# Kernel optimization log

Measured on AMD Instinct MI355X. Metric: run time of the kernel, lower is better.

## Reference

```python
import jax, jax.numpy as jnp
import numpy as np
from itertools import product

L0 = (41, 1600, 1408)  # sparse_shape (z,y,x) from pc_range / voxel_size + [1,0,0]
B = 4
N_PER = 25000
PNAMES = ['w_in','s_in','b_in','w1','s1','b1','w2a','s2a','b2a','w2b','s2b','b2b','w2c','s2c','b2c','w3a','s3a','b3a','w3b','s3b','b3b','w3c','s3c','b3c','w4a','s4a','b4a','w4b','s4b','b4b','w4c','s4c','b4c','w_out','s_out','b_out']


def _enc(c, shape):
    D, H, W = shape
    return ((c[:, 0].astype(np.int64) * D + c[:, 1]) * H + c[:, 2]) * W + c[:, 3]


def _subm_rb(coords, shape):
    # submanifold conv rulebook: out site i gathers input j with coord_j = coord_i + offset
    N = coords.shape[0]
    keys = _enc(coords, shape)
    order = np.argsort(keys); sk = keys[order]
    ins, outs = [], []
    for dz, dy, dx in product((-1, 0, 1), repeat=3):
        nb = coords.astype(np.int64).copy()
        nb[:, 1] += dz; nb[:, 2] += dy; nb[:, 3] += dx
        ok = ((nb[:, 1] >= 0) & (nb[:, 1] < shape[0]) & (nb[:, 2] >= 0) & (nb[:, 2] < shape[1]) & (nb[:, 3] >= 0) & (nb[:, 3] < shape[2]))
        qi = np.nonzero(ok)[0]
        qk = _enc(nb[qi], shape)
        pos = np.clip(np.searchsorted(sk, qk), 0, N - 1)
        f = sk[pos] == qk
        ins.append(order[pos[f]].astype(np.int32))
        outs.append(qi[f].astype(np.int32))
    R = max(len(a) for a in ins)
    rin = np.zeros((27, R), np.int32); rout = np.full((27, R), N, np.int32)  # pad -> dummy out row
    for k in range(27):
        rin[k, :len(ins[k])] = ins[k]; rout[k, :len(outs[k])] = outs[k]
    return jnp.asarray(rin), jnp.asarray(rout)


def _spconv_rb(coords, shape, ks, st, pd):
    # strided sparse conv: out = (in + pad - k) / stride where divisible and in-bounds
    osh = tuple((shape[i] + 2 * pd[i] - ks[i]) // st[i] + 1 for i in range(3))
    per = []; allk = []
    for off in product(*[range(k) for k in ks]):
        oc = np.empty((coords.shape[0], 4), np.int64)
        oc[:, 0] = coords[:, 0]
        ok = np.ones(coords.shape[0], bool)
        for d in range(3):
            v = coords[:, d + 1].astype(np.int64) + pd[d] - off[d]
            ok &= (v % st[d] == 0)
            v = v // st[d]
            ok &= (v >= 0) & (v < osh[d])
            oc[:, d + 1] = v
        qi = np.nonzero(ok)[0]
        qk = _enc(oc[qi], osh)
        per.append((qi.astype(np.int32), qk)); allk.append(qk)
    uk = np.unique(np.concatenate(allk))
    Nout = len(uk); K = len(per)
    R = max(len(qi) for qi, _ in per)
    rin = np.zeros((K, R), np.int32); rout = np.full((K, R), Nout, np.int32)
    for k, (qi, qk) in enumerate(per):
        rin[k, :len(qi)] = qi
        rout[k, :len(qi)] = np.searchsorted(uk, qk).astype(np.int32)
    t = uk.copy()
    x = t % osh[2]; t //= osh[2]; y = t % osh[1]; t //= osh[1]; z = t % osh[0]; b = t // osh[0]
    ocoords = np.stack([b, z, y, x], 1).astype(np.int32)
    return jnp.asarray(rin), jnp.asarray(rout), ocoords, osh


def _gen_coords(rng):
    # clustered LiDAR-like voxel occupancy: gaussian clusters so 3x3x3 neighborhoods are populated
    out = []
    for b in range(B):
        nc = 250
        ctr = np.stack([rng.integers(6, 34, nc), rng.integers(60, 1540, nc), rng.integers(60, 1348, nc)], 1)
        pts = ctr[np.repeat(np.arange(nc), 400)] + rng.normal(0.0, 2.0, (nc * 400, 3))
        pts = np.rint(pts).astype(np.int64)
        for d in range(3):
            pts[:, d] = np.clip(pts[:, d], 0, L0[d] - 1)
        keys = (pts[:, 0] * L0[1] + pts[:, 1]) * L0[2] + pts[:, 2]
        _, ui = np.unique(keys, return_index=True)
        assert len(ui) >= N_PER
        c = pts[np.sort(ui[:N_PER])]
        out.append(np.concatenate([np.full((N_PER, 1), b, np.int64), c], 1))
    return np.concatenate(out, 0).astype(np.int32)


def _conv(feat, W, rin, rout, nout):
    # gather -> per-offset GEMM -> scatter-add (spconv rulebook algorithm)
    out = jnp.zeros((nout + 1, W.shape[2]), feat.dtype)  # +1 dummy row for padding
    for k in range(W.shape[0]):
        out = out.at[rout[k]].add(feat[rin[k]] @ W[k])
    return out[:nout]


def _bnrelu(x, s, b):
    # eval-mode BatchNorm1d folded to affine, then ReLU
    return jax.nn.relu(x * s + b)


def _net(voxels, normalizer, rb1_in, rb1_out, rb2s_in, rb2s_out, batch2, rb2_in, rb2_out, rb3s_in, rb3s_out, batch3, rb3_in, rb3_out, rb4s_in, rb4s_out, batch4, rb4_in, rb4_out, rbo_in, rbo_out, batch_out, P):
    n0 = voxels.shape[0]; n2 = batch2.shape[0]; n3 = batch3.shape[0]; n4 = batch4.shape[0]; no = batch_out.shape[0]
    f = voxels.sum(1) / normalizer  # mean VFE: (N0, 4)
    x = _bnrelu(_conv(f, P['w_in'], rb1_in, rb1_out, n0), P['s_in'], P['b_in'])
    x = _bnrelu(_conv(x, P['w1'], rb1_in, rb1_out, n0), P['s1'], P['b1'])
    x = _bnrelu(_conv(x, P['w2a'], rb2s_in, rb2s_out, n2), P['s2a'], P['b2a'])
    x = _bnrelu(_conv(x, P['w2b'], rb2_in, rb2_out, n2), P['s2b'], P['b2b'])
    x = _bnrelu(_conv(x, P['w2c'], rb2_in, rb2_out, n2), P['s2c'], P['b2c'])
    x = _bnrelu(_conv(x, P['w3a'], rb3s_in, rb3s_out, n3), P['s3a'], P['b3a'])
    x = _bnrelu(_conv(x, P['w3b'], rb3_in, rb3_out, n3), P['s3b'], P['b3b'])
    x = _bnrelu(_conv(x, P['w3c'], rb3_in, rb3_out, n3), P['s3c'], P['b3c'])
    x = _bnrelu(_conv(x, P['w4a'], rb4s_in, rb4s_out, n4), P['s4a'], P['b4a'])
    x = _bnrelu(_conv(x, P['w4b'], rb4_in, rb4_out, n4), P['s4b'], P['b4b'])
    x = _bnrelu(_conv(x, P['w4c'], rb4_in, rb4_out, n4), P['s4c'], P['b4c'])
    x = _bnrelu(_conv(x, P['w_out'], rbo_in, rbo_out, no), P['s_out'], P['b_out'])
    # per-batch global max pool over active voxels (== F.max_pool1d over voxel dim)
    return jax.ops.segment_max(x, batch_out.astype(jnp.int32), num_segments=B)


def setup_inputs():
    rng = np.random.default_rng(0)
    coords0 = _gen_coords(rng)
    rb1_in, rb1_out = _subm_rb(coords0, L0)
    rb2s_in, rb2s_out, c2, sh2 = _spconv_rb(coords0, L0, (3, 3, 3), (2, 2, 2), (1, 1, 1))
    rb2_in, rb2_out = _subm_rb(c2, sh2)
    rb3s_in, rb3s_out, c3, sh3 = _spconv_rb(c2, sh2, (3, 3, 3), (2, 2, 2), (1, 1, 1))
    rb3_in, rb3_out = _subm_rb(c3, sh3)
    rb4s_in, rb4s_out, c4, sh4 = _spconv_rb(c3, sh3, (3, 3, 3), (2, 2, 2), (0, 1, 1))
    rb4_in, rb4_out = _subm_rb(c4, sh4)
    rbo_in, rbo_out, co, _ = _spconv_rb(c4, sh4, (3, 1, 1), (2, 1, 1), (0, 0, 0))
    N0 = coords0.shape[0]
    d = dict(
        voxels=jnp.asarray(rng.normal(0, 1, (N0, 5, 4)).astype(np.float32)),
        voxel_num_points=jnp.asarray(rng.integers(1, 6, N0).astype(np.int32)),
        voxel_coords=jnp.asarray(coords0),
        rb1_in=rb1_in, rb1_out=rb1_out,
        rb2s_in=rb2s_in, rb2s_out=rb2s_out, batch2=jnp.asarray(c2[:, 0]),
        rb2_in=rb2_in, rb2_out=rb2_out,
        rb3s_in=rb3s_in, rb3s_out=rb3s_out, batch3=jnp.asarray(c3[:, 0]),
        rb3_in=rb3_in, rb3_out=rb3_out,
        rb4s_in=rb4s_in, rb4s_out=rb4s_out, batch4=jnp.asarray(c4[:, 0]),
        rb4_in=rb4_in, rb4_out=rb4_out,
        rbo_in=rbo_in, rbo_out=rbo_out, batch_out=jnp.asarray(co[:, 0]),
    )
    def _w(k, ci, co_):
        return jnp.asarray((rng.normal(0, 1, (k, ci, co_)) / np.sqrt(k * ci)).astype(np.float32))
    def _bn(c):
        return (jnp.asarray(rng.uniform(0.5, 1.5, c).astype(np.float32)), jnp.asarray(rng.normal(0, 0.1, c).astype(np.float32)))
    d['w_in'] = _w(27, 4, 16); d['s_in'], d['b_in'] = _bn(16)
    d['w1'] = _w(27, 16, 16); d['s1'], d['b1'] = _bn(16)
    d['w2a'] = _w(27, 16, 32); d['s2a'], d['b2a'] = _bn(32)
    d['w2b'] = _w(27, 32, 32); d['s2b'], d['b2b'] = _bn(32)
    d['w2c'] = _w(27, 32, 32); d['s2c'], d['b2c'] = _bn(32)
    d['w3a'] = _w(27, 32, 64); d['s3a'], d['b3a'] = _bn(64)
    d['w3b'] = _w(27, 64, 64); d['s3b'], d['b3b'] = _bn(64)
    d['w3c'] = _w(27, 64, 64); d['s3c'], d['b3c'] = _bn(64)
    d['w4a'] = _w(27, 64, 64); d['s4a'], d['b4a'] = _bn(64)
    d['w4b'] = _w(27, 64, 64); d['s4b'], d['b4b'] = _bn(64)
    d['w4c'] = _w(27, 64, 64); d['s4c'], d['b4c'] = _bn(64)
    d['w_out'] = _w(3, 64, 128); d['s_out'], d['b_out'] = _bn(128)
    return d


def reference(voxels, voxel_num_points, voxel_coords, rb1_in, rb1_out, rb2s_in, rb2s_out, batch2, rb2_in, rb2_out, rb3s_in, rb3s_out, batch3, rb3_in, rb3_out, rb4s_in, rb4s_out, batch4, rb4_in, rb4_out, rbo_in, rbo_out, batch_out, w_in, s_in, b_in, w1, s1, b1, w2a, s2a, b2a, w2b, s2b, b2b, w2c, s2c, b2c, w3a, s3a, b3a, w3b, s3b, b3b, w3c, s3c, b3c, w4a, s4a, b4a, w4b, s4b, b4b, w4c, s4c, b4c, w_out, s_out, b_out):
    normalizer = jnp.maximum(voxel_num_points.astype(voxels.dtype), 1.0)[:, None]
    P = dict(zip(PNAMES, (w_in, s_in, b_in, w1, s1, b1, w2a, s2a, b2a, w2b, s2b, b2b, w2c, s2c, b2c, w3a, s3a, b3a, w3b, s3b, b3b, w3c, s3c, b3c, w4a, s4a, b4a, w4b, s4b, b4b, w4c, s4c, b4c, w_out, s_out, b_out)))
    return _net(voxels, normalizer, rb1_in, rb1_out, rb2s_in, rb2s_out, batch2, rb2_in, rb2_out, rb3s_in, rb3s_out, batch3, rb3_in, rb3_out, rb4s_in, rb4s_out, batch4, rb4_in, rb4_out, rbo_in, rbo_out, batch_out, P)
```

## Files before the change

kernel.cpp:

```cpp
#include <hip/hip_runtime.h>
#include <cstddef>
#include <cstdint>

typedef _Float16 half8 __attribute__((ext_vector_type(8)));
typedef float floatx4 __attribute__((ext_vector_type(4)));

static inline int cdiv_i(int a, int b) { return (a + b - 1) / b; }

__global__ void feat_kernel(const float* __restrict__ vox,
                            const int* __restrict__ vnp,
                            _Float16* __restrict__ f, int N0) {
  int t = blockIdx.x * blockDim.x + threadIdx.x;
  if (t >= (N0 + 1) * 8) return;
  int i = t >> 3, c = t & 7;
  float v = 0.f;
  if (i < N0 && c < 4) {
    const float* p = vox + (size_t)i * 20 + c;
    v = (p[0] + p[4] + p[8] + p[12] + p[16]) / fmaxf((float)vnp[i], 1.f);
  }
  f[t] = (_Float16)v;
}

struct RB { const int* rin; const int* rout; int K, R, nout, start, end, off; };
struct RBs { RB d[8]; };
__global__ void rb_fill_all(RBs P, int* __restrict__ tbl, int total) {
  int idx = blockIdx.x * blockDim.x + threadIdx.x;
  if (idx >= total) return;
#pragma unroll
  for (int l = 0; l < 8; ++l) {
    if (idx >= P.d[l].start && idx < P.d[l].end) {
      const RB rb = P.d[l];
      int e = idx - rb.start;
      int o = rb.rout[e];
      if ((unsigned)o < (unsigned)rb.nout) {
        int k = e / rb.R;
        tbl[rb.off + (size_t)k * rb.nout + o] = rb.rin[e];
      }
    }
  }
}

__global__ void tbl_fill_kernel(const int* __restrict__ rin,
                                const int* __restrict__ rout,
                                int* __restrict__ tbl, int K, int R, int nout) {
  int e = blockIdx.x * blockDim.x + threadIdx.x;
  if (e >= K * R) return;
  int o = rout[e];
  if ((unsigned)o >= (unsigned)nout) return;
  int k = e / R;
  tbl[(size_t)k * nout + o] = rin[e];
}

struct WP { const float* W; int K, Ci, CiPad, Co, start, end, off; };
struct WPs { WP d[12]; };
__global__ void wpack_all(WPs P, _Float16* __restrict__ Bp, int total) {
  int idx = blockIdx.x * blockDim.x + threadIdx.x;
  if (idx >= total) return;
#pragma unroll
  for (int l = 0; l < 12; ++l) {
    if (idx >= P.d[l].start && idx < P.d[l].end) {
      const WP w = P.d[l];
      int e = idx - w.start;
      int j = e & 7;
      int lane = (e >> 3) & 63;
      int rest = e >> 9;
      int NT = w.Co >> 4;
      int t = rest % NT, ch = rest / NT;
      int kk = ch * 32 + ((lane >> 4) << 3) + j;
      int k = kk / w.CiPad, ci = kk % w.CiPad;
      int n = t * 16 + (lane & 15);
      float v = (k < w.K && ci < w.Ci)
                    ? w.W[((size_t)k * w.Ci + ci) * w.Co + n]
                    : 0.f;
      Bp[w.off + e] = (_Float16)v;
    }
  }
}

template <int K, int CiPad, int Co, int KS, int CG, int CBLK>
__global__ __launch_bounds__(256) void conv_mfma(
    const _Float16* __restrict__ feat, const _Float16* __restrict__ Bp,
    const int* __restrict__ tbl, const float* __restrict__ sc,
    const float* __restrict__ bi, _Float16* __restrict__ out,
    int nout, int nin) {
  constexpr int NT = Co / 16;
  constexpr int NTE = NT / CBLK;
  constexpr int NTW = NTE / CG;
  constexpr int RG = 4 / (KS * CG);
  static_assert(KS * CG * RG == 4 && RG >= 1 && NT % CBLK == 0 && NTE % CG == 0);
  constexpr int DIV = (CiPad >= 32) ? (CiPad / 32) : 1;
  constexpr int NCH = (K * CiPad + 31) / 32;
  constexpr int L2C = (CiPad == 8) ? 3 : 4;
  constexpr int CoP = NTE * 16 + 4;

  __shared__ float red[(KS > 1) ? (KS - 1) * RG * 16 * CoP : 1];

  if (blockIdx.x == 0 && threadIdx.x < Co)
    out[(size_t)nout * Co + threadIdx.x] = (_Float16)0.f;

  int id = blockIdx.x;
  {
    int nb = gridDim.x, nb8 = (nb >> 3) << 3;
    if (id < nb8) {
      int per = nb >> 3;
      id = (id & 7) * per + (id >> 3);
    }
  }
  const int rt = id / CBLK, cb = id % CBLK;

  const int wave = threadIdx.x >> 6, lane = threadIdx.x & 63;
  const int ks = wave % KS;
  const int cg = (wave / KS) % CG;
  const int rowg = wave / (KS * CG);
  const int m = lane & 15, lb = (lane >> 4) * 8;
  const int i0 = (rt * RG + rowg) * 16;
  if constexpr (KS == 1) {
    if (i0 >= nout) return;
  }
  const int row = i0 + m;
  const bool rOK = row < nout;
  const int ct0 = cb * NTE + cg * NTW;

  floatx4 acc[NTW];
#pragma unroll
  for (int n = 0; n < NTW; ++n) {
    floatx4 z = {0.f, 0.f, 0.f, 0.f};
    acc[n] = z;
  }

  if constexpr (CiPad >= 32) {
    constexpr int NKW = (K + KS - 1) / KS;
    constexpr int NC = NKW * DIV;
    constexpr int DA = NC < 8 ? NC : 8;
    constexpr int DB = NC < 2 ? NC : 2;
    int idx[NKW];
#pragma unroll
    for (int q = 0; q < NKW; ++q) {
      int k = ks + q * KS;
      int jj = (rOK && k < K) ? tbl[(size_t)k * nout + row] : -1;
      idx[q] = (jj < 0) ? nin : jj;
    }
    half8 ap[DA];
    half8 bq[DB][NTW];
#pragma unroll
    for (int d = 0; d < DA; ++d)
      ap[d] = *(const half8*)(feat + (size_t)idx[d / DIV] * CiPad +
                              (d % DIV) * 32 + lb);
#pragma unroll
    for (int d = 0; d < DB; ++d) {
      int k = ks + (d / DIV) * KS;
      int ch = ((k < K) ? k : (K - 1)) * DIV + (d % DIV);
#pragma unroll
      for (int n = 0; n < NTW; ++n)
        bq[d][n] = *(const half8*)(Bp + ((size_t)ch * NT * 64 + lane) * 8 +
                                   (size_t)(ct0 + n) * 512);
    }
#pragma unroll
    for (int ii = 0; ii < NC; ++ii) {
      half8 a = ap[ii % DA];
      half8 bt[NTW];
#pragma unroll
      for (int n = 0; n < NTW; ++n) bt[n] = bq[ii % DB][n];
      if (ii + DA < NC) {
        int nx = ii + DA;
        ap[ii % DA] = *(const half8*)(feat + (size_t)idx[nx / DIV] * CiPad +
                                      (nx % DIV) * 32 + lb);
      }
      if (ii + DB < NC) {
        int nx = ii + DB;
        int k = ks + (nx / DIV) * KS;
        int ch = ((k < K) ? k : (K - 1)) * DIV + (nx % DIV);
#pragma unroll
        for (int n = 0; n < NTW; ++n)
          bq[ii % DB][n] = *(const half8*)(Bp + ((size_t)ch * NT * 64 + lane) * 8 +
                                           (size_t)(ct0 + n) * 512);
      }
#pragma unroll
      for (int n = 0; n < NTW; ++n)
        acc[n] = __builtin_amdgcn_mfma_f32_16x16x32_f16(a, bt[n], acc[n], 0, 0, 0);
    }
  } else {
    constexpr int NCW = (NCH + KS - 1) / KS;
    constexpr int DA = NCW < 8 ? NCW : 8;
    constexpr int DB = NCW < 2 ? NCW : 2;
    int idx[NCW];
#pragma unroll
    for (int q = 0; q < NCW; ++q) {
      int ch = ks + q * KS;
      int ko = (ch * 32 + lb) >> L2C;
      int jj = (rOK && ko < K && ch < NCH) ? tbl[(size_t)ko * nout + row] : -1;
      idx[q] = (jj < 0) ? nin : jj;
    }
    half8 ap[DA];
    half8 bq[DB][NTW];
#pragma unroll
    for (int d = 0; d < DA; ++d) {
      int ch = ks + d * KS;
      ap[d] = *(const half8*)(feat + (size_t)idx[d] * CiPad +
                              ((ch * 32 + lb) & (CiPad - 1)));
    }
#pragma unroll
    for (int d = 0; d < DB; ++d) {
      int ch = ks + d * KS;
      if (ch >= NCH) ch = NCH - 1;
#pragma unroll
      for (int n = 0; n < NTW; ++n)
        bq[d][n] = *(const half8*)(Bp + ((size_t)ch * NT * 64 + lane) * 8 +
                                   (size_t)(ct0 + n) * 512);
    }
#pragma unroll
    for (int ii = 0; ii < NCW; ++ii) {
      half8 a = ap[ii % DA];
      half8 bt[NTW];
#pragma unroll
      for (int n = 0; n < NTW; ++n) bt[n] = bq[ii % DB][n];
      if (ii + DA < NCW) {
        int nx = ii + DA;
        int ch = ks + nx * KS;
        ap[ii % DA] = *(const half8*)(feat + (size_t)idx[nx] * CiPad +
                                      ((ch * 32 + lb) & (CiPad - 1)));
      }
      if (ii + DB < NCW) {
        int nx = ii + DB;
        int ch = ks + nx * KS;
        if (ch >= NCH) ch = NCH - 1;
#pragma unroll
        for (int n = 0; n < NTW; ++n)
          bq[ii % DB][n] = *(const half8*)(Bp + ((size_t)ch * NT * 64 + lane) * 8 +
                                           (size_t)(ct0 + n) * 512);
      }
#pragma unroll
      for (int n = 0; n < NTW; ++n)
        acc[n] = __builtin_amdgcn_mfma_f32_16x16x32_f16(a, bt[n], acc[n], 0, 0, 0);
    }
  }

  const int rl = (lane >> 4) * 4;
  if constexpr (KS > 1) {
    if (ks > 0) {
#pragma unroll
      for (int n = 0; n < NTW; ++n) {
        int lcol = (cg * NTW + n) * 16 + m;
#pragma unroll
        for (int r = 0; r < 4; ++r)
          red[((ks - 1) * RG + rowg) * 16 * CoP + (rl + r) * CoP + lcol] = acc[n][r];
      }
    }
    __syncthreads();
    if (ks > 0) return;
#pragma unroll
    for (int s = 1; s < KS; ++s)
#pragma unroll
      for (int n = 0; n < NTW; ++n) {
        int lcol = (cg * NTW + n) * 16 + m;
#pragma unroll
        for (int r = 0; r < 4; ++r)
          acc[n][r] += red[((s - 1) * RG + rowg) * 16 * CoP + (rl + r) * CoP + lcol];
      }
  }

#pragma unroll
  for (int n = 0; n < NTW; ++n) {
    int col = (ct0 + n) * 16 + m;
    float s_ = sc[col], b_ = bi[col];
#pragma unroll
    for (int r = 0; r < 4; ++r) {
      int orow = i0 + rl + r;
      if (orow < nout)
        out[(size_t)orow * Co + col] = (_Float16)fmaxf(fmaf(acc[n][r], s_, b_), 0.f);
    }
  }
}

__global__ __launch_bounds__(256) void segmax2(const _Float16* __restrict__ x,
                                               const int* __restrict__ batch,
                                               int n, float* __restrict__ out) {
  const int RPB = 128;
  int c = threadIdx.x & 127, g = threadIdx.x >> 7;
  int r0 = blockIdx.x * RPB + g;
  int rend = min(n, blockIdx.x * RPB + RPB);
  float mx = 0.f;
  int cb = -1;
  for (int r = r0; r < rend; r += 2) {
    int b = batch[r];
    if (b != cb) {
      if (cb >= 0)
        atomicMax((int*)out + ((size_t)cb << 7) + c, __float_as_int(mx));
      cb = b;
      mx = 0.f;
    }
    mx = fmaxf(mx, (float)x[(size_t)r * 128 + c]);
  }
  if (cb >= 0)
    atomicMax((int*)out + ((size_t)cb << 7) + c, __float_as_int(mx));
}

extern "C" void kernel_launch(void* const* d_in, const int* in_sizes, int n_in,
                              void* d_out, int out_size, void* d_ws, size_t ws_size,
                              hipStream_t stream) {
  auto I = [&](int idx) { return (const int*)d_in[idx]; };
  auto F = [&](int idx) { return (const float*)d_in[idx]; };

  const int N0  = in_sizes[1];
  const int R1  = in_sizes[3] / 27;
  const int R2s = in_sizes[5] / 27;
  const int n2  = in_sizes[7];
  const int R2  = in_sizes[8] / 27;
  const int R3s = in_sizes[10] / 27;
  const int n3  = in_sizes[12];
  const int R3  = in_sizes[13] / 27;
  const int R4s = in_sizes[15] / 27;
  const int n4  = in_sizes[17];
  const int R4  = in_sizes[18] / 27;
  const int Ro  = in_sizes[20] / 3;
  const int no  = in_sizes[22];

  const int wIdx[12] = {23, 26, 29, 32, 35, 38, 41, 44, 47, 50, 53, 56};
  const int Ks[12]   = {27, 27, 27, 27, 27, 27, 27, 27, 27, 27, 27, 3};
  const int Cis[12]  = {4, 16, 16, 32, 32, 32, 64, 64, 64, 64, 64, 64};
  const int Cos[12]  = {16, 16, 32, 32, 32, 64, 64, 64, 64, 64, 64, 128};
  WPs P;
  int wtot = 0;
  int bpOff[12];
  for (int l = 0; l < 12; ++l) {
    int cip = Cis[l] < 8 ? 8 : Cis[l];
    int nch = (Ks[l] * cip + 31) / 32;
    int nt = Cos[l] / 16;
    int sz = nch * nt * 512;
    P.d[l].W = F(wIdx[l]);
    P.d[l].K = Ks[l];  P.d[l].Ci = Cis[l];  P.d[l].CiPad = cip;  P.d[l].Co = Cos[l];
    P.d[l].start = wtot;  P.d[l].end = wtot + sz;  P.d[l].off = wtot;
    bpOff[l] = wtot;
    wtot += sz;
  }

  RBs RP;
  const int rbRin[8]  = {3, 5, 8, 10, 13, 15, 18, 20};
  const int rbRs[8]   = {R1, R2s, R2, R3s, R3, R4s, R4, Ro};
  const int rbKs[8]   = {27, 27, 27, 27, 27, 27, 27, 3};
  const int rbNout[8] = {N0, n2, n2, n3, n3, n4, n4, no};
  size_t tblInts[8], tblOff[8];
  size_t totTbl = 0;
  int totFill = 0;
  for (int l = 0; l < 8; ++l) {
    tblInts[l] = (size_t)rbNout[l] * rbKs[l];
    tblOff[l] = totTbl;
    totTbl += tblInts[l];
    RP.d[l].rin = I(rbRin[l]);
    RP.d[l].rout = I(rbRin[l] + 1);
    RP.d[l].K = rbKs[l];  RP.d[l].R = rbRs[l];  RP.d[l].nout = rbNout[l];
    RP.d[l].start = totFill;
    totFill += rbKs[l] * rbRs[l];
    RP.d[l].end = totFill;
    RP.d[l].off = (int)tblOff[l];
  }

  size_t S = (size_t)(N0 + 1) * 16;
  auto smax = [&](size_t v) { if (v > S) S = v; };
  smax((size_t)(n2 + 1) * 32);
  smax((size_t)(n3 + 1) * 64);
  smax((size_t)(n4 + 1) * 64);
  smax((size_t)(no + 1) * 128);
  S = (S + 7) & ~(size_t)7;

  _Float16* h = (_Float16*)d_ws;
  size_t off = 0;
  _Float16* f0 = h + off;   off += (size_t)(N0 + 1) * 8;
  _Float16* bufA = h + off; off += S;
  _Float16* bufB = h + off; off += S;
  _Float16* Bp = h + off;   off += (size_t)((wtot + 7) & ~7);
  int* tblBase = (int*)(h + off);
  size_t usedBytes = off * 2;
  bool prebuilt = (usedBytes + totTbl * 4 <= ws_size);

  feat_kernel<<<cdiv_i((N0 + 1) * 8, 256), 256, 0, stream>>>(F(0), I(1), f0, N0);
  wpack_all<<<cdiv_i(wtot, 256), 256, 0, stream>>>(P, Bp, wtot);
  hipMemsetAsync(d_out, 0, (size_t)out_size * 4, stream);

  const int l2rb[12] = {0, 0, 1, 2, 2, 3, 4, 4, 5, 6, 6, 7};
  const int* tblL[12];
  if (prebuilt) {
    hipMemsetAsync(tblBase, 0xFF, totTbl * 4, stream);
    rb_fill_all<<<cdiv_i(totFill, 256), 256, 0, stream>>>(RP, tblBase, totFill);
    for (int l = 0; l < 12; ++l) tblL[l] = tblBase + tblOff[l2rb[l]];
  } else {
    for (int l = 0; l < 12; ++l) tblL[l] = tblBase;
  }
  auto buildSeq = [&](int rb) {
    if (prebuilt) return;
    hipMemsetAsync(tblBase, 0xFF, tblInts[rb] * 4, stream);
    tbl_fill_kernel<<<cdiv_i(rbKs[rb] * rbRs[rb], 256), 256, 0, stream>>>(
        I(rbRin[rb]), I(rbRin[rb] + 1), tblBase, rbKs[rb], rbRs[rb], rbNout[rb]);
  };

#define CONV(Kk, CIP, CO, KSv, CGv, CBv, IN, LI, OUTB, NOUT, NIN)             \
  do {                                                                        \
    constexpr int rowsPerBlk = (4 / (KSv * CGv)) * 16;                        \
    int nblk = cdiv_i(NOUT, rowsPerBlk) * CBv;                                \
    conv_mfma<Kk, CIP, CO, KSv, CGv, CBv>                                     \
        <<<nblk, 256, 0, stream>>>(                                           \
            IN, Bp + bpOff[LI], tblL[LI], F(wIdx[LI] + 1), F(wIdx[LI] + 2),   \
            OUTB, NOUT, NIN);                                                 \
  } while (0)

  buildSeq(0);
  CONV(27, 8, 16, 1, 1, 1, f0, 0, bufA, N0, N0);
  CONV(27, 16, 16, 2, 1, 1, bufA, 1, bufB, N0, N0);
  buildSeq(1);
  CONV(27, 16, 32, 2, 1, 1, bufB, 2, bufA, n2, N0);
  buildSeq(2);
  CONV(27, 32, 32, 2, 1, 1, bufA, 3, bufB, n2, n2);
  CONV(27, 32, 32, 2, 1, 1, bufB, 4, bufA, n2, n2);
  buildSeq(3);
  CONV(27, 32, 64, 4, 1, 1, bufA, 5, bufB, n3, n2);
  buildSeq(4);
  CONV(27, 64, 64, 4, 1, 1, bufB, 6, bufA, n3, n3);
  CONV(27, 64, 64, 4, 1, 1, bufA, 7, bufB, n3, n3);
  buildSeq(5);
  CONV(27, 64, 64, 4, 1, 2, bufB, 8, bufA, n4, n3);
  buildSeq(6);
  CONV(27, 64, 64, 4, 1, 2, bufA, 9, bufB, n4, n4);
  CONV(27, 64, 64, 4, 1, 2, bufB, 10, bufA, n4, n4);
  buildSeq(7);
  CONV(3, 64, 128, 2, 2, 2, bufA, 11, bufB, no, n4);
  segmax2<<<cdiv_i(no, 128), 256, 0, stream>>>(bufB, I(22), no, (float*)d_out);
#undef CONV
}
```

Measured before the change: 448.2 us.

## Use 32x32x16 MFMA conv kernel with repacked weights for mid layers

Adds a conv_mfma32 kernel that uses 32x32x16 f16 MFMA tiles (32 rows per wave) plus a matching 32-column weight packing, and switches layers 3-10 to it with new K-split/column-group configurations. Larger MFMA tiles raise arithmetic per loaded A/B fragment and cut the number of instructions per output. In exchange they use more accumulator registers and LDS for the K-split reduction, and give coarser row tiles on sparse row counts.

After: 451.2 us. No clear change (+0.7%).

```diff
diff --git a/kernel.cpp b/kernel.cpp
--- a/kernel.cpp
+++ b/kernel.cpp
@@ -4,6 +4,7 @@
 
 typedef _Float16 half8 __attribute__((ext_vector_type(8)));
 typedef float floatx4 __attribute__((ext_vector_type(4)));
+typedef float floatx16 __attribute__((ext_vector_type(16)));
 
 static inline int cdiv_i(int a, int b) { return (a + b - 1) / b; }
 
@@ -51,7 +52,7 @@
   tbl[(size_t)k * nout + o] = rin[e];
 }
 
-struct WP { const float* W; int K, Ci, CiPad, Co, start, end, off; };
+struct WP { const float* W; int K, Ci, CiPad, Co, start, end, off, p32; };
 struct WPs { WP d[12]; };
 __global__ void wpack_all(WPs P, _Float16* __restrict__ Bp, int total) {
   int idx = blockIdx.x * blockDim.x + threadIdx.x;
@@ -64,14 +65,23 @@
       int j = e & 7;
       int lane = (e >> 3) & 63;
       int rest = e >> 9;
-      int NT = w.Co >> 4;
-      int t = rest % NT, ch = rest / NT;
-      int kk = ch * 32 + ((lane >> 4) << 3) + j;
-      int k = kk / w.CiPad, ci = kk % w.CiPad;
-      int n = t * 16 + (lane & 15);
-      float v = (k < w.K && ci < w.Ci)
-                    ? w.W[((size_t)k * w.Ci + ci) * w.Co + n]
-                    : 0.f;
+      float v;
+      if (w.p32) {
+        int NT = w.Co >> 5;
+        int t = rest % NT, ch = rest / NT;
+        int SUB = w.CiPad >> 4;
+        int ko = ch / SUB, s = ch % SUB;
+        int ci = s * 16 + ((lane >> 5) << 3) + j;
+        int col = t * 32 + (lane & 31);
+        v = w.W[((size_t)ko * w.Ci + ci) * w.Co + col];
+      } else {
+        int NT = w.Co >> 4;
+        int t = rest % NT, ch = rest / NT;
+        int kk = ch * 32 + ((lane >> 4) << 3) + j;
+        int k = kk / w.CiPad, ci = kk % w.CiPad;
+        int n = t * 16 + (lane & 15);
+        v = (k < w.K && ci < w.Ci) ? w.W[((size_t)k * w.Ci + ci) * w.Co + n] : 0.f;
+      }
       Bp[w.off + e] = (_Float16)v;
     }
   }
@@ -88,9 +98,9 @@
   constexpr int NTW = NTE / CG;
   constexpr int RG = 4 / (KS * CG);
   static_assert(KS * CG * RG == 4 && RG >= 1 && NT % CBLK == 0 && NTE % CG == 0);
-  constexpr int DIV = (CiPad >= 32) ? (CiPad / 32) : 1;
   constexpr int NCH = (K * CiPad + 31) / 32;
   constexpr int L2C = (CiPad == 8) ? 3 : 4;
+  constexpr int DIV = (CiPad >= 32) ? (CiPad / 32) : 1;
   constexpr int CoP = NTE * 16 + 4;
 
   __shared__ float red[(KS > 1) ? (KS - 1) * RG * 16 * CoP : 1];
@@ -99,34 +109,23 @@
     out[(size_t)nout * Co + threadIdx.x] = (_Float16)0.f;
 
   int id = blockIdx.x;
-  {
-    int nb = gridDim.x, nb8 = (nb >> 3) << 3;
-    if (id < nb8) {
-      int per = nb >> 3;
-      id = (id & 7) * per + (id >> 3);
-    }
-  }
+  { int nb = gridDim.x, nb8 = (nb >> 3) << 3;
+    if (id < nb8) { int per = nb >> 3; id = (id & 7) * per + (id >> 3); } }
   const int rt = id / CBLK, cb = id % CBLK;
-
   const int wave = threadIdx.x >> 6, lane = threadIdx.x & 63;
   const int ks = wave % KS;
   const int cg = (wave / KS) % CG;
   const int rowg = wave / (KS * CG);
   const int m = lane & 15, lb = (lane >> 4) * 8;
   const int i0 = (rt * RG + rowg) * 16;
-  if constexpr (KS == 1) {
-    if (i0 >= nout) return;
-  }
+  if constexpr (KS == 1) { if (i0 >= nout) return; }
   const int row = i0 + m;
   const bool rOK = row < nout;
   const int ct0 = cb * NTE + cg * NTW;
 
   floatx4 acc[NTW];
 #pragma unroll
-  for (int n = 0; n < NTW; ++n) {
-    floatx4 z = {0.f, 0.f, 0.f, 0.f};
-    acc[n] = z;
-  }
+  for (int n = 0; n < NTW; ++n) { floatx4 z = {0,0,0,0}; acc[n] = z; }
 
   if constexpr (CiPad >= 32) {
     constexpr int NKW = (K + KS - 1) / KS;
@@ -140,12 +139,10 @@
       int jj = (rOK && k < K) ? tbl[(size_t)k * nout + row] : -1;
       idx[q] = (jj < 0) ? nin : jj;
     }
-    half8 ap[DA];
-    half8 bq[DB][NTW];
+    half8 ap[DA]; half8 bq[DB][NTW];
 #pragma unroll
     for (int d = 0; d < DA; ++d)
-      ap[d] = *(const half8*)(feat + (size_t)idx[d / DIV] * CiPad +
-                              (d % DIV) * 32 + lb);
+      ap[d] = *(const half8*)(feat + (size_t)idx[d / DIV] * CiPad + (d % DIV) * 32 + lb);
 #pragma unroll
     for (int d = 0; d < DB; ++d) {
       int k = ks + (d / DIV) * KS;
@@ -191,13 +188,11 @@
       int jj = (rOK && ko < K && ch < NCH) ? tbl[(size_t)ko * nout + row] : -1;
       idx[q] = (jj < 0) ? nin : jj;
     }
-    half8 ap[DA];
-    half8 bq[DB][NTW];
+    half8 ap[DA]; half8 bq[DB][NTW];
 #pragma unroll
     for (int d = 0; d < DA; ++d) {
       int ch = ks + d * KS;
-      ap[d] = *(const half8*)(feat + (size_t)idx[d] * CiPad +
-                              ((ch * 32 + lb) & (CiPad - 1)));
+      ap[d] = *(const half8*)(feat + (size_t)idx[d] * CiPad + ((ch * 32 + lb) & (CiPad - 1)));
     }
 #pragma unroll
     for (int d = 0; d < DB; ++d) {
@@ -268,6 +263,134 @@
       int orow = i0 + rl + r;
       if (orow < nout)
         out[(size_t)orow * Co + col] = (_Float16)fmaxf(fmaf(acc[n][r], s_, b_), 0.f);
+    }
+  }
+}
+
+template <int K, int CiPad, int Co, int KS, int CG, int CBLK>
+__global__ __launch_bounds__(256) void conv_mfma32(
+    const _Float16* __restrict__ feat, const _Float16* __restrict__ Bp,
+    const int* __restrict__ tbl, const float* __restrict__ sc,
+    const float* __restrict__ bi, _Float16* __restrict__ out,
+    int nout, int nin) {
+  constexpr int NT = Co / 32;
+  constexpr int NTE = NT / CBLK;
+  constexpr int NTW = NTE / CG;
+  constexpr int RG = 4 / (KS * CG);
+  static_assert(KS * CG * RG == 4 && RG >= 1 && NT % CBLK == 0 && NTE % CG == 0 && NTW >= 1);
+  constexpr int SUB = CiPad / 16;
+  constexpr int NKW = (K + KS - 1) / KS;
+  constexpr int NC = NKW * SUB;
+  constexpr int DA = NC < 8 ? NC : 8;
+  constexpr int DB = NC < 2 ? NC : 2;
+  constexpr int CoP = NTE * 32 + 4;
+
+  __shared__ float red[(KS > 1) ? (KS - 1) * RG * 32 * CoP : 1];
+
+  if (blockIdx.x == 0 && threadIdx.x < Co)
+    out[(size_t)nout * Co + threadIdx.x] = (_Float16)0.f;
+
+  int id = blockIdx.x;
+  { int nb = gridDim.x, nb8 = (nb >> 3) << 3;
+    if (id < nb8) { int per = nb >> 3; id = (id & 7) * per + (id >> 3); } }
+  const int rt = id / CBLK, cb = id % CBLK;
+  const int wave = threadIdx.x >> 6, lane = threadIdx.x & 63;
+  const int ks = wave % KS;
+  const int cg = (wave / KS) % CG;
+  const int rowg = wave / (KS * CG);
+  const int m = lane & 31, lb = (lane >> 5) * 8, h = lane >> 5;
+  const int i0 = (rt * RG + rowg) * 32;
+  if constexpr (KS == 1) { if (i0 >= nout) return; }
+  const int row = i0 + m;
+  const bool rOK = row < nout;
+  const int ct0 = cb * NTE + cg * NTW;
+
+  floatx16 acc[NTW];
+#pragma unroll
+  for (int n = 0; n < NTW; ++n)
+#pragma unroll
+    for (int r = 0; r < 16; ++r) acc[n][r] = 0.f;
+
+  int idx[NKW];
+#pragma unroll
+  for (int q = 0; q < NKW; ++q) {
+    int k = ks + q * KS;
+    int jj = (rOK && k < K) ? tbl[(size_t)k * nout + row] : -1;
+    idx[q] = (jj < 0) ? nin : jj;
+  }
+
+  half8 ap[DA]; half8 bq[DB][NTW];
+#pragma unroll
+  for (int d = 0; d < DA; ++d)
+    ap[d] = *(const half8*)(feat + (size_t)idx[d / SUB] * CiPad + (d % SUB) * 16 + lb);
+#pragma unroll
+  for (int d = 0; d < DB; ++d) {
+    int k = ks + (d / SUB) * KS;
+    int ch = ((k < K) ? k : (K - 1)) * SUB + (d % SUB);
+#pragma unroll
+    for (int n = 0; n < NTW; ++n)
+      bq[d][n] = *(const half8*)(Bp + (size_t)(ch * NT + ct0 + n) * 512 + lane * 8);
+  }
+#pragma unroll
+  for (int ii = 0; ii < NC; ++ii) {
+    half8 a = ap[ii % DA];
+    half8 bt[NTW];
+#pragma unroll
+    for (int n = 0; n < NTW; ++n) bt[n] = bq[ii % DB][n];
+    if (ii + DA < NC) {
+      int nx = ii + DA;
+      ap[ii % DA] = *(const half8*)(feat + (size_t)idx[nx / SUB] * CiPad +
+                                    (nx % SUB) * 16 + lb);
+    }
+    if (ii + DB < NC) {
+      int nx = ii + DB;
+      int k = ks + (nx / SUB) * KS;
+      int ch = ((k < K) ? k : (K - 1)) * SUB + (nx % SUB);
+#pragma unroll
+      for (int n = 0; n < NTW; ++n)
+        bq[ii % DB][n] = *(const half8*)(Bp + (size_t)(ch * NT + ct0 + n) * 512 + lane * 8);
+    }
+#pragma unroll
+    for (int n = 0; n < NTW; ++n)
+      acc[n] = __builtin_amdgcn_mfma_f32_32x32x16_f16(a, bt[n], acc[n], 0, 0, 0);
+  }
+
+  if constexpr (KS > 1) {
+    if (ks > 0) {
+#pragma unroll
+      for (int n = 0; n < NTW; ++n) {
+        int lcol = (cg * NTW + n) * 32 + m;
+#pragma unroll
+        for (int reg = 0; reg < 16; ++reg) {
+          int r = (reg & 3) + 8 * (reg >> 2) + 4 * h;
+          red[((ks - 1) * RG + rowg) * 32 * CoP + r * CoP + lcol] = acc[n][reg];
+        }
+      }
+    }
+    __syncthreads();
+    if (ks > 0) return;
+#pragma unroll
+    for (int s = 1; s < KS; ++s)
+#pragma unroll
+      for (int n = 0; n < NTW; ++n) {
+        int lcol = (cg * NTW + n) * 32 + m;
+#pragma unroll
+        for (int reg = 0; reg < 16; ++reg) {
+          int r = (reg & 3) + 8 * (reg >> 2) + 4 * h;
+          acc[n][reg] += red[((s - 1) * RG + rowg) * 32 * CoP + r * CoP + lcol];
+        }
+      }
+  }
+
+#pragma unroll
+  for (int n = 0; n < NTW; ++n) {
+    int col = (ct0 + n) * 32 + m;
+    float s_ = sc[col], b_ = bi[col];
+#pragma unroll
+    for (int reg = 0; reg < 16; ++reg) {
+      int orow = i0 + (reg & 3) + 8 * (reg >> 2) + 4 * h;
+      if (orow < nout)
+        out[(size_t)orow * Co + col] = (_Float16)fmaxf(fmaf(acc[n][reg], s_, b_), 0.f);
     }
   }
 }
@@ -284,15 +407,12 @@
   for (int r = r0; r < rend; r += 2) {
     int b = batch[r];
     if (b != cb) {
-      if (cb >= 0)
-        atomicMax((int*)out + ((size_t)cb << 7) + c, __float_as_int(mx));
-      cb = b;
-      mx = 0.f;
+      if (cb >= 0) atomicMax((int*)out + ((size_t)cb << 7) + c, __float_as_int(mx));
+      cb = b; mx = 0.f;
     }
     mx = fmaxf(mx, (float)x[(size_t)r * 128 + c]);
   }
-  if (cb >= 0)
-    atomicMax((int*)out + ((size_t)cb << 7) + c, __float_as_int(mx));
+  if (cb >= 0) atomicMax((int*)out + ((size_t)cb << 7) + c, __float_as_int(mx));
 }
 
 extern "C" void kernel_launch(void* const* d_in, const int* in_sizes, int n_in,
@@ -319,17 +439,18 @@
   const int Ks[12]   = {27, 27, 27, 27, 27, 27, 27, 27, 27, 27, 27, 3};
   const int Cis[12]  = {4, 16, 16, 32, 32, 32, 64, 64, 64, 64, 64, 64};
   const int Cos[12]  = {16, 16, 32, 32, 32, 64, 64, 64, 64, 64, 64, 128};
+  const int P32[12]  = {0, 0, 0, 1, 1, 1, 1, 1, 1, 1, 1, 0};
   WPs P;
   int wtot = 0;
   int bpOff[12];
   for (int l = 0; l < 12; ++l) {
     int cip = Cis[l] < 8 ? 8 : Cis[l];
-    int nch = (Ks[l] * cip + 31) / 32;
-    int nt = Cos[l] / 16;
-    int sz = nch * nt * 512;
+    int sz;
+    if (P32[l]) sz = Ks[l] * (cip / 16) * (Cos[l] / 32) * 512;
+    else        sz = ((Ks[l] * cip + 31) / 32) * (Cos[l] / 16) * 512;
     P.d[l].W = F(wIdx[l]);
-    P.d[l].K = Ks[l];  P.d[l].Ci = Cis[l];  P.d[l].CiPad = cip;  P.d[l].Co = Cos[l];
-    P.d[l].start = wtot;  P.d[l].end = wtot + sz;  P.d[l].off = wtot;
+    P.d[l].K = Ks[l]; P.d[l].Ci = Cis[l]; P.d[l].CiPad = cip; P.d[l].Co = Cos[l];
+    P.d[l].start = wtot; P.d[l].end = wtot + sz; P.d[l].off = wtot; P.d[l].p32 = P32[l];
     bpOff[l] = wtot;
     wtot += sz;
   }
@@ -348,7 +469,7 @@
     totTbl += tblInts[l];
     RP.d[l].rin = I(rbRin[l]);
     RP.d[l].rout = I(rbRin[l] + 1);
-    RP.d[l].K = rbKs[l];  RP.d[l].R = rbRs[l];  RP.d[l].nout = rbNout[l];
+    RP.d[l].K = rbKs[l]; RP.d[l].R = rbRs[l]; RP.d[l].nout = rbNout[l];
     RP.d[l].start = totFill;
     totFill += rbKs[l] * rbRs[l];
     RP.d[l].end = totFill;
@@ -393,36 +514,44 @@
         I(rbRin[rb]), I(rbRin[rb] + 1), tblBase, rbKs[rb], rbRs[rb], rbNout[rb]);
   };
 
-#define CONV(Kk, CIP, CO, KSv, CGv, CBv, IN, LI, OUTB, NOUT, NIN)             \
+#define CONV16(Kk, CIP, CO, KSv, CGv, CBv, IN, LI, OUTB, NOUT, NIN)           \
   do {                                                                        \
     constexpr int rowsPerBlk = (4 / (KSv * CGv)) * 16;                        \
     int nblk = cdiv_i(NOUT, rowsPerBlk) * CBv;                                \
-    conv_mfma<Kk, CIP, CO, KSv, CGv, CBv>                                     \
-        <<<nblk, 256, 0, stream>>>(                                           \
-            IN, Bp + bpOff[LI], tblL[LI], F(wIdx[LI] + 1), F(wIdx[LI] + 2),   \
-            OUTB, NOUT, NIN);                                                 \
+    conv_mfma<Kk, CIP, CO, KSv, CGv, CBv><<<nblk, 256, 0, stream>>>(          \
+        IN, Bp + bpOff[LI], tblL[LI], F(wIdx[LI] + 1), F(wIdx[LI] + 2),       \
+        OUTB, NOUT, NIN);                                                     \
   } while (0)
+#define CONV32(Kk, CIP, CO, KSv, CGv, CBv, IN, LI, OUTB, NOUT, NIN)           \
+  do {                                                                        \
+    constexpr int rowsPerBlk = (4 / (KSv * CGv)) * 32;                        \
+    int nblk = cdiv_i(NOUT, rowsPerBlk) * CBv;                                \
+    conv_mfma32<Kk, CIP, CO, KSv, CGv, CBv><<<nblk, 256, 0, stream>>>(        \
+        IN, Bp + bpOff[LI], tblL[LI], F(wIdx[LI] + 1), F(wIdx[LI] + 2),       \
+        OUTB, NOUT, NIN);                                                     \
+  } while (0)
 
   buildSeq(0);
-  CONV(27, 8, 16, 1, 1, 1, f0, 0, bufA, N0, N0);
-  CONV(27, 16, 16, 2, 1, 1, bufA, 1, bufB, N0, N0);
+  CONV16(27, 8, 16, 1, 1, 1, f0, 0, bufA, N0, N0);
+  CONV16(27, 16, 16, 2, 1, 1, bufA, 1, bufB, N0, N0);
   buildSeq(1);
-  CONV(27, 16, 32, 2, 1, 1, bufB, 2, bufA, n2, N0);
+  CONV16(27, 16, 32, 2, 1, 1, bufB, 2, bufA, n2, N0);
   buildSeq(2);
-  CONV(27, 32, 32, 2, 1, 1, bufA, 3, bufB, n2, n2);
-  CONV(27, 32, 32, 2, 1, 1, bufB, 4, bufA, n2, n2);
+  CONV32(27, 32, 32, 4, 1, 1, bufA, 3, bufB, n2, n2);
+  CONV32(27, 32, 32, 4, 1, 1, bufB, 4, bufA, n2, n2);
   buildSeq(3);
-  CONV(27, 32, 64, 4, 1, 1, bufA, 5, bufB, n3, n2);
+  CONV32(27, 32, 64, 2, 2, 1, bufA, 5, bufB, n3, n2);
   buildSeq(4);
-  CONV(27, 64, 64, 4, 1, 1, bufB, 6, bufA, n3, n3);
-  CONV(27, 64, 64, 4, 1, 1, bufA, 7, bufB, n3, n3);
+  CONV32(27, 64, 64, 2, 2, 1, bufB, 6, bufA, n3, n3);
+  CONV32(27, 64, 64, 2, 2, 1, bufA, 7, bufB, n3, n3);
   buildSeq(5);
-  CONV(27, 64, 64, 4, 1, 2, bufB, 8, bufA, n4, n3);
+  CONV32(27, 64, 64, 4, 1, 2, bufB, 8, bufA, n4, n3);
   buildSeq(6);
-  CONV(27, 64, 64, 4, 1, 2, bufA, 9, bufB, n4, n4);
-  CONV(27, 64, 64, 4, 1, 2, bufB, 10, bufA, n4, n4);
+  CONV32(27, 64, 64, 4, 1, 2, bufA, 9, bufB, n4, n4);
+  CONV32(27, 64, 64, 4, 1, 2, bufB, 10, bufA, n4, n4);
   buildSeq(7);
-  CONV(3, 64, 128, 2, 2, 2, bufA, 11, bufB, no, n4);
+  CONV16(3, 64, 128, 2, 2, 2, bufA, 11, bufB, no, n4);
   segmax2<<<cdiv_i(no, 128), 256, 0, stream>>>(bufB, I(22), no, (float*)d_out);
-#undef CONV
-}
+#undef CONV16
+#undef CONV32
+}
```
